# Kernel tuning notes

Hardware: AMD Instinct MI355X
Metric: run time of the kernel (lower is better)

Reference implementation:

```python
import jax, jax.numpy as jnp
import numpy as np

CHUNK = 128  # time_chunk_size from init_kwargs
EPS = 1e-8


def _forward(v, k, alpha, q):
    # v: (T,B,d), k/alpha/q: (T,B,n)
    T, B, d = v.shape
    n = k.shape[-1]
    nc = T // CHUNK  # T assumed divisible by CHUNK
    vr = v.reshape(nc, CHUNK, B, d)
    kr = k.reshape(nc, CHUNK, B, n)
    ar = alpha.reshape(nc, CHUNK, B, n)
    qr = q.reshape(nc, CHUNK, B, n)

    def step(S_prev, xs):
        vc, kc, ac, qc = xs  # (C,B,d), (C,B,n), ...
        outer = jnp.einsum('tbd,tbn->tbdn', vc, kc)          # (C,B,d,n)
        log_a = jnp.log(jnp.clip(ac, EPS))
        log_cp = jnp.cumsum(log_a, axis=0)                   # (C,B,n)
        cp = jnp.exp(log_cp)
        decay = cp / (cp[-1:] + EPS)                         # normalized per chunk
        S_local = jnp.cumsum(outer * decay[:, :, None, :], axis=0)
        prefix = jnp.exp(log_cp[0])                          # (B,n) decay of first step
        S_local = S_local + (S_prev * prefix[:, None, :])[None]
        y = jnp.einsum('tbdn,tbn->tbd', S_local, qc)         # (C,B,d)
        return S_local[-1], y

    S0 = jnp.zeros((B, d, n), v.dtype)
    _, ys = jax.lax.scan(step, S0, (vr, kr, ar, qr))
    return ys.reshape(T, B, d)


def setup_inputs() -> dict:
    key = jax.random.key(0)
    k1, k2, k3, k4 = jax.random.split(key, 4)
    T, B, d, n = 2048, 4, 256, 256
    return {
        'v': jax.random.normal(k1, (T, B, d), jnp.float32),
        'k': jax.random.normal(k2, (T, B, n), jnp.float32),
        'alpha': jax.random.uniform(k3, (T, B, n), jnp.float32),
        'q': jax.random.normal(k4, (T, B, n), jnp.float32),
    }


def reference(v, k, alpha, q):
    return _forward(v, k, alpha, q)
```

## Files before the change

### kernel.cpp

```cpp
#include <hip/hip_runtime.h>
#include <math.h>

typedef unsigned short u16;
typedef unsigned int u32;
typedef __bf16 bf16x8 __attribute__((ext_vector_type(8)));
typedef float f32x4 __attribute__((ext_vector_type(4)));

#define BB   4
#define DD   256
#define NN   256
#define CH   128
#define NCH  16
#define EPSF 1e-8f

#define WS_QB  0u
#define WS_VT  (4u<<20)
#define WS_WT  (8u<<20)
#define WS_WN  (12u<<20)
#define WS_AST (16u<<20)
#define WS_SPT (18u<<20)
#define WS_PF  (26u<<20)
#define WS_UT  (28u<<20)

__device__ __forceinline__ u16 f2bf(float x) {
  u32 u = __float_as_uint(x);
  u32 r = (u + 0x7fffu + ((u >> 16) & 1u)) >> 16;
  return (u16)r;
}
__device__ __forceinline__ float bf2f(u32 lo16) {
  return __uint_as_float(lo16 << 16);
}

__device__ __forceinline__ int xcd_swz(int bid, int nwg) {
  return (bid & 7) * (nwg >> 3) + (bid >> 3);
}

__device__ __forceinline__ void gload16(void* lds, const void* g) {
  __builtin_amdgcn_global_load_lds((const __attribute__((address_space(1))) void*)g,
                                   (__attribute__((address_space(3))) void*)lds, 16, 0, 0);
}

__device__ __forceinline__ void stage_tile(u16* lds, const u16* g, int rowstride) {
  int tid = threadIdx.x;
#pragma unroll
  for (int h = 0; h < 2; h++) {
    int ci = tid + h * 256;
    int r = ci >> 3, sl = ci & 7;
    const u16* src = g + (size_t)r * rowstride + ((sl ^ (r & 7)) << 3);
    gload16(lds + (size_t)ci * 8, src);
  }
}

__device__ __forceinline__ void read_frags(const u16* buf, int rbase, int lane,
                                           bf16x8 (&f)[2][2]) {
#pragma unroll
  for (int i = 0; i < 2; i++)
#pragma unroll
    for (int ks = 0; ks < 2; ks++) {
      int r = rbase + i * 16 + (lane & 15);
      int slot = ((ks << 2) + (lane >> 4)) ^ (r & 7);
      f[i][ks] = *reinterpret_cast<const bf16x8*>(buf + r * 64 + slot * 8);
    }
}

__device__ __forceinline__ void mma_step(const u16* Ab, const u16* Bb, int rm, int cn,
                                         int lane, f32x4 (&acc)[2][2]) {
  bf16x8 a[2][2], b[2][2];
  read_frags(Ab, rm, lane, a);
  read_frags(Bb, cn, lane, b);
#pragma unroll
  for (int mf = 0; mf < 2; mf++)
#pragma unroll
    for (int nf = 0; nf < 2; nf++)
#pragma unroll
      for (int ks = 0; ks < 2; ks++)
        acc[mf][nf] = __builtin_amdgcn_mfma_f32_16x16x32_bf16(a[mf][ks], b[nf][ks],
                                                              acc[mf][nf], 0, 0, 0);
}

__global__ __launch_bounds__(256) void k_prep(const float* __restrict__ q,
                                              const float* __restrict__ v,
                                              const float* __restrict__ kin,
                                              const float* __restrict__ alpha,
                                              u16* __restrict__ qb,
                                              u16* __restrict__ vT,
                                              u16* __restrict__ wT,
                                              u16* __restrict__ wn,
                                              float* __restrict__ pf) {
  __shared__ __align__(16) char smem[64 * 136 * 2];
  int bid = blockIdx.x;
  int tid = threadIdx.x;
  if (bid < 1024) {
    int ng = bid & 15, b = (bid >> 4) & 3, c = bid >> 6;
    int nn = tid & 15, seg = tid >> 4;
    int n = ng * 16 + nn;
    int cb = c * BB + b;
    const int stride = BB * NN;
    size_t gbase = ((size_t)(c * CH + seg * 8) * stride) + b * NN + n;
    float lg[8], kv[8];
    float a0 = 0.f, run = 0.f;
#pragma unroll
    for (int i = 0; i < 8; i++) {
      float av = fmaxf(alpha[gbase + (size_t)i * stride], EPSF);
      kv[i] = kin[gbase + (size_t)i * stride];
      if (i == 0) a0 = av;
      run += __logf(av);
      lg[i] = run;
    }
    float (*tot)[17] = (float(*)[17])smem;
    tot[seg][nn] = run;
    __syncthreads();
    float prefix = 0.f, total = 0.f;
#pragma unroll
    for (int j = 0; j < 16; j++) {
      float tv = tot[j][nn];
      if (j < seg) prefix += tv;
      total += tv;
    }
    float rden = 1.f / (__expf(total) + EPSF);
    union { u16 u[8]; uint4 v4; } pk;
    u16* wnrow = wn + (size_t)cb * (CH * NN) + n;
#pragma unroll
    for (int i = 0; i < 8; i++) {
      float cp = __expf(prefix + lg[i]);
      u16 h = f2bf(kv[i] * (cp * rden));
      pk.u[i] = h;
      wnrow[(size_t)(seg * 8 + i) * NN] = h;
    }
    *(uint4*)(wT + (size_t)cb * (NN * CH) + (size_t)n * CH + seg * 8) = pk.v4;
    if (seg == 0) pf[cb * NN + n] = a0;
  } else if (bid < 1280) {
    int b2 = bid - 1024;
    int dt = b2 & 3, cb = b2 >> 2;
    int c = cb >> 2, b = cb & 3;
    int d0 = dt * 64;
    u16* vt = (u16*)smem;
    int sr = tid >> 4, chd = tid & 15;
#pragma unroll
    for (int p = 0; p < 8; p++) {
      int s = p * 16 + sr;
      float4 x = *(const float4*)&v[((size_t)(c * CH + s) * BB + b) * DD + d0 + chd * 4];
      int dbase = chd * 4;
      vt[(dbase + 0) * 136 + s] = f2bf(x.x);
      vt[(dbase + 1) * 136 + s] = f2bf(x.y);
      vt[(dbase + 2) * 136 + s] = f2bf(x.z);
      vt[(dbase + 3) * 136 + s] = f2bf(x.w);
    }
    __syncthreads();
    int dr = tid >> 2, ch = tid & 3;
    const uint4* srcl = (const uint4*)&vt[dr * 136 + ch * 32];
    uint4 a0 = srcl[0], a1 = srcl[1], a2 = srcl[2], a3 = srcl[3];
    uint4* dst = (uint4*)&vT[((size_t)cb * DD + d0 + dr) * CH + ch * 32];
    dst[0] = a0; dst[1] = a1; dst[2] = a2; dst[3] = a3;
  } else {
    size_t gid = (size_t)(bid - 1280) * 256 + tid;
    const float4* src = (const float4*)q + gid * 2;
    float4 x = src[0], z = src[1];
    union { u16 u[8]; uint4 v4; } pk;
    pk.u[0] = f2bf(x.x); pk.u[1] = f2bf(x.y); pk.u[2] = f2bf(x.z); pk.u[3] = f2bf(x.w);
    pk.u[4] = f2bf(z.x); pk.u[5] = f2bf(z.y); pk.u[6] = f2bf(z.z); pk.u[7] = f2bf(z.w);
    ((uint4*)qb)[gid] = pk.v4;
  }
}

__global__ __launch_bounds__(256) void k_ut(const u16* __restrict__ vT,
                                            const u16* __restrict__ wT,
                                            u16* __restrict__ utb) {
  __shared__ u16 Al[2][4096], Bl[2][4096];
  int bid = xcd_swz(blockIdx.x, 1024);
  int tid = threadIdx.x, lane = tid & 63, wv = tid >> 6;
  int rm = (wv >> 1) * 32, cn = (wv & 1) * 32;
  int nt = bid & 3, dt = (bid >> 2) & 3, cb = bid >> 4;
  const u16* A = vT + ((size_t)cb * DD + dt * 64) * CH;
  const u16* B = wT + ((size_t)cb * NN + nt * 64) * CH;
  f32x4 acc[2][2] = {};
  stage_tile(Al[0], A, CH); stage_tile(Al[1], A + 64, CH);
  stage_tile(Bl[0], B, CH); stage_tile(Bl[1], B + 64, CH);
  __syncthreads();
  mma_step(Al[0], Bl[0], rm, cn, lane, acc);
  mma_step(Al[1], Bl[1], rm, cn, lane, acc);
  u16* out = utb + ((size_t)cb * DD + dt * 64) * NN + nt * 64;
#pragma unroll
  for (int mf = 0; mf < 2; mf++)
#pragma unroll
    for (int nf = 0; nf < 2; nf++)
#pragma unroll
      for (int r = 0; r < 4; r++) {
        int row = rm + mf * 16 + (lane >> 4) * 4 + r;
        int col = cn + nf * 16 + (lane & 15);
        out[(size_t)row * NN + col] = f2bf(acc[mf][nf][r]);
      }
}

__global__ __launch_bounds__(256) void k_scanas(const u16* __restrict__ qb,
                                                const u16* __restrict__ wn,
                                                const u32* __restrict__ utT2,
                                                const float* __restrict__ pf,
                                                u16* __restrict__ asT,
                                                u32* __restrict__ sptT2) {
  __shared__ u16 Al[2][4096], Bl[2][4096];
  int bid = blockIdx.x;
  int tid = threadIdx.x;
  if (bid < 192) {
    int lane = tid & 63, wv = tid >> 6;
    int rm = (wv >> 1) * 32, cn = (wv & 1) * 32;
    int tile = bid % 3;
    int cb = bid / 3;
    int ti = (tile == 0) ? 0 : 1;
    int si = (tile == 2) ? 1 : 0;
    int t0 = ti * 64, s0 = si * 64;
    int c = cb >> 2, b = cb & 3;
    const u16* A = qb + ((size_t)(c * CH + t0) * BB + b) * NN;
    const u16* B = wn + (size_t)cb * (CH * NN) + (size_t)s0 * NN;
    f32x4 acc[2][2] = {};
    stage_tile(Al[0], A, BB * NN); stage_tile(Bl[0], B, NN);
    __syncthreads();
    for (int st = 0; st < 4; st++) {
      int nx = st + 1;
      if (nx < 4) {
        stage_tile(Al[nx & 1], A + nx * 64, BB * NN);
        stage_tile(Bl[nx & 1], B + nx * 64, NN);
      }
      mma_step(Al[st & 1], Bl[st & 1], rm, cn, lane, acc);
      __syncthreads();
    }
    u16* outb = asT + (size_t)cb * (CH * CH);
#pragma unroll
    for (int mf = 0; mf < 2; mf++)
#pragma unroll
      for (int nf = 0; nf < 2; nf++)
#pragma unroll
        for (int r = 0; r < 4; r++) {
          int t = t0 + rm + mf * 16 + (lane >> 4) * 4 + r;
          int s = s0 + cn + nf * 16 + (lane & 15);
          float val = (s <= t) ? acc[mf][nf][r] : 0.f;
          outb[(size_t)t * CH + s] = f2bf(val);
        }
  } else {
    int id = (bid - 192) * 256 + tid;
    int nh = id & 127, dd = (id >> 7) & 255, b = id >> 15;
    u32 u[NCH];
    float2 pp[NCH];
#pragma unroll
    for (int ch = 0; ch < NCH; ch++) {
      int cb = ch * BB + b;
      u[ch] = utT2[((size_t)cb * DD + dd) * 128 + nh];
      pp[ch] = *(const float2*)&pf[cb * NN + nh * 2];
    }
    float S0 = 0.f, S1 = 0.f;
#pragma unroll
    for (int ch = 0; ch < NCH; ch++) {
      int cb = ch * BB + b;
      float Sp0 = S0 * pp[ch].x, Sp1 = S1 * pp[ch].y;
      sptT2[((size_t)cb * DD + dd) * 128 + nh] = (u32)f2bf(Sp0) | ((u32)f2bf(Sp1) << 16);
      S0 = Sp0 + bf2f(u[ch] & 0xffffu);
      S1 = Sp1 + bf2f(u[ch] >> 16);
    }
  }
}

__global__ __launch_bounds__(256) void k_out(const u16* __restrict__ qb,
                                             const u16* __restrict__ sptT,
                                             const u16* __restrict__ asT,
                                             const u16* __restrict__ vT,
                                             float* __restrict__ y) {
  int bid = xcd_swz(blockIdx.x, 512);
  int dt = bid & 3, tt = (bid >> 2) & 1, cb = bid >> 3;
  int c = cb >> 2, b = cb & 3;
  int t0 = tt * 64, d0 = dt * 64;
  int tid = threadIdx.x, lane = tid & 63, wv = tid >> 6;
  int rm = (wv >> 1) * 32, cn = (wv & 1) * 32;
  const u16* A1 = qb + ((size_t)(c * CH + t0) * BB + b) * NN;
  const u16* B1 = sptT + ((size_t)cb * DD + d0) * NN;
  const u16* A2 = asT + (size_t)cb * (CH * CH) + (size_t)t0 * CH;
  const u16* B2 = vT + ((size_t)cb * DD + d0) * CH;
  __shared__ u16 Al[2][4096], Bl[2][4096];
  f32x4 acc[2][2] = {};
  int nst = 5 + tt;
  stage_tile(Al[0], A1, BB * NN); stage_tile(Bl[0], B1, NN);
  __syncthreads();
  for (int st = 0; st < nst; st++) {
    int nx = st + 1;
    if (nx < 4) {
      stage_tile(Al[nx & 1], A1 + nx * 64, BB * NN);
      stage_tile(Bl[nx & 1], B1 + nx * 64, NN);
    } else if (nx < nst) {
      stage_tile(Al[nx & 1], A2 + (nx - 4) * 64, CH);
      stage_tile(Bl[nx & 1], B2 + (nx - 4) * 64, CH);
    }
    mma_step(Al[st & 1], Bl[st & 1], rm, cn, lane, acc);
    __syncthreads();
  }
  float* out = y + ((size_t)(c * CH + t0) * BB + b) * DD + d0;
#pragma unroll
  for (int mf = 0; mf < 2; mf++)
#pragma unroll
    for (int nf = 0; nf < 2; nf++)
#pragma unroll
      for (int r = 0; r < 4; r++) {
        int row = rm + mf * 16 + (lane >> 4) * 4 + r;
        int col = cn + nf * 16 + (lane & 15);
        out[(size_t)row * (BB * DD) + col] = acc[mf][nf][r];
      }
}

extern "C" void kernel_launch(void* const* d_in, const int* in_sizes, int n_in,
                              void* d_out, int out_size, void* d_ws, size_t ws_size,
                              hipStream_t stream) {
  const float* v = (const float*)d_in[0];
  const float* k = (const float*)d_in[1];
  const float* alpha = (const float*)d_in[2];
  const float* q = (const float*)d_in[3];
  float* y = (float*)d_out;
  char* ws = (char*)d_ws;
  u16* qb = (u16*)(ws + WS_QB);
  u16* vT = (u16*)(ws + WS_VT);
  u16* wT = (u16*)(ws + WS_WT);
  u16* wn = (u16*)(ws + WS_WN);
  u16* asT = (u16*)(ws + WS_AST);
  u16* sptT = (u16*)(ws + WS_SPT);
  float* pf = (float*)(ws + WS_PF);
  u16* utb = (u16*)(ws + WS_UT);

  k_prep<<<2304, 256, 0, stream>>>(q, v, k, alpha, qb, vT, wT, wn, pf);
  k_ut<<<1024, 256, 0, stream>>>(vT, wT, utb);
  k_scanas<<<704, 256, 0, stream>>>(qb, wn, (const u32*)utb, pf, asT, (u32*)sptT);
  k_out<<<512, 256, 0, stream>>>(qb, sptT, asT, vT, y);
}
```

Measured before the change: 35.79 us.

## Deepen LDS staging pipelines in scan and output GEMM kernels

In k_scanas, all four K-tiles are staged into LDS up front behind a single barrier, so the per-step barriers go away. In k_out, the double buffer becomes a triple buffer with prefetch distance two, using explicit vmcnt waits and raw s_barrier instead of __syncthreads. The aim is to keep more global loads in flight and cut synchronisation stalls. The cost is more LDS per block (64KB and 48KB), which may lower occupancy. The hand-set vmcnt values assume stage_tile issues a fixed number of loads per call, and the output stays correct only if that holds.

```diff
diff --git a/kernel.cpp b/kernel.cpp
--- a/kernel.cpp
+++ b/kernel.cpp
@@ -198,7 +198,7 @@
                                                 const float* __restrict__ pf,
                                                 u16* __restrict__ asT,
                                                 u32* __restrict__ sptT2) {
-  __shared__ u16 Al[2][4096], Bl[2][4096];
+  __shared__ u16 Al[4][4096], Bl[4][4096];
   int bid = blockIdx.x;
   int tid = threadIdx.x;
   if (bid < 192) {
@@ -213,17 +213,15 @@
     const u16* A = qb + ((size_t)(c * CH + t0) * BB + b) * NN;
     const u16* B = wn + (size_t)cb * (CH * NN) + (size_t)s0 * NN;
     f32x4 acc[2][2] = {};
-    stage_tile(Al[0], A, BB * NN); stage_tile(Bl[0], B, NN);
+#pragma unroll
+    for (int p = 0; p < 4; p++) {
+      stage_tile(Al[p], A + p * 64, BB * NN);
+      stage_tile(Bl[p], B + p * 64, NN);
+    }
     __syncthreads();
-    for (int st = 0; st < 4; st++) {
-      int nx = st + 1;
-      if (nx < 4) {
-        stage_tile(Al[nx & 1], A + nx * 64, BB * NN);
-        stage_tile(Bl[nx & 1], B + nx * 64, NN);
-      }
-      mma_step(Al[st & 1], Bl[st & 1], rm, cn, lane, acc);
-      __syncthreads();
-    }
+#pragma unroll
+    for (int p = 0; p < 4; p++)
+      mma_step(Al[p], Bl[p], rm, cn, lane, acc);
     u16* outb = asT + (size_t)cb * (CH * CH);
 #pragma unroll
     for (int mf = 0; mf < 2; mf++)
@@ -274,23 +272,40 @@
   const u16* B1 = sptT + ((size_t)cb * DD + d0) * NN;
   const u16* A2 = asT + (size_t)cb * (CH * CH) + (size_t)t0 * CH;
   const u16* B2 = vT + ((size_t)cb * DD + d0) * CH;
-  __shared__ u16 Al[2][4096], Bl[2][4096];
+  __shared__ u16 Al[3][4096], Bl[3][4096];
   f32x4 acc[2][2] = {};
   int nst = 5 + tt;
-  stage_tile(Al[0], A1, BB * NN); stage_tile(Bl[0], B1, NN);
-  __syncthreads();
+
+#define STG_OUT(s)                                                   \
+  do {                                                               \
+    if ((s) < 4) {                                                   \
+      stage_tile(Al[(s) % 3], A1 + (s) * 64, BB * NN);               \
+      stage_tile(Bl[(s) % 3], B1 + (s) * 64, NN);                    \
+    } else {                                                         \
+      stage_tile(Al[(s) % 3], A2 + ((s) - 4) * 64, CH);              \
+      stage_tile(Bl[(s) % 3], B2 + ((s) - 4) * 64, CH);              \
+    }                                                                \
+  } while (0)
+
+  STG_OUT(0);
+  STG_OUT(1);
+  asm volatile("s_waitcnt vmcnt(4)" ::: "memory");
+  __builtin_amdgcn_sched_barrier(0);
+  __builtin_amdgcn_s_barrier();
+
   for (int st = 0; st < nst; st++) {
-    int nx = st + 1;
-    if (nx < 4) {
-      stage_tile(Al[nx & 1], A1 + nx * 64, BB * NN);
-      stage_tile(Bl[nx & 1], B1 + nx * 64, NN);
-    } else if (nx < nst) {
-      stage_tile(Al[nx & 1], A2 + (nx - 4) * 64, CH);
-      stage_tile(Bl[nx & 1], B2 + (nx - 4) * 64, CH);
-    }
-    mma_step(Al[st & 1], Bl[st & 1], rm, cn, lane, acc);
-    __syncthreads();
+    bool more = (st + 2 < nst);
+    if (more) STG_OUT(st + 2);
+    mma_step(Al[st % 3], Bl[st % 3], rm, cn, lane, acc);
+    if (st + 1 < nst) {
+      if (more) asm volatile("s_waitcnt vmcnt(4)" ::: "memory");
+      else      asm volatile("s_waitcnt vmcnt(0)" ::: "memory");
+      __builtin_amdgcn_sched_barrier(0);
+      __builtin_amdgcn_s_barrier();
+    }
   }
+#undef STG_OUT
+
   float* out = y + ((size_t)(c * CH + t0) * BB + b) * DD + d0;
 #pragma unroll
   for (int mf = 0; mf < 2; mf++)
```

Measured after the change: 35.86 us. Within noise of the previous version (+0.2%).
